# Kernel tuning notes

Hardware: AMD Instinct MI355X
Metric: run time of the kernel (lower is better)

The kernel has to match this reference:

```python
import jax, jax.numpy as jnp
import numpy as np

N_NODES = 50000
N_EDGES = 800000
IN_CH = 128
HID = 256
HEADS = 4
NEG_SLOPE = 0.2


def setup_inputs() -> dict:
    key = jax.random.key(0)
    ks = jax.random.split(key, 12)
    C1 = HID // HEADS  # 64 per head, layer 1
    inp = {
        "x": jax.random.normal(ks[0], (N_NODES, IN_CH), dtype=jnp.float32),
        "edge_index": jax.random.randint(ks[1], (2, N_EDGES), 0, N_NODES, dtype=jnp.int32),
        # layer 1: GATConv(128 -> 64, heads=4, concat=True)
        "W1": jax.random.normal(ks[2], (IN_CH, HEADS * C1), dtype=jnp.float32) * (1.0 / np.sqrt(IN_CH)),
        "a_src1": jax.random.normal(ks[3], (HEADS, C1), dtype=jnp.float32) * 0.1,
        "a_dst1": jax.random.normal(ks[4], (HEADS, C1), dtype=jnp.float32) * 0.1,
        "b1": jnp.zeros((HEADS * C1,), dtype=jnp.float32),
        # layer 2: GATConv(256 -> 256, heads=1, concat=False)
        "W2": jax.random.normal(ks[5], (HID, HID), dtype=jnp.float32) * (1.0 / np.sqrt(HID)),
        "a_src2": jax.random.normal(ks[6], (1, HID), dtype=jnp.float32) * 0.1,
        "a_dst2": jax.random.normal(ks[7], (1, HID), dtype=jnp.float32) * 0.1,
        "b2": jnp.zeros((HID,), dtype=jnp.float32),
    }
    return inp


def _gat_conv(x, src, dst, W, a_src, a_dst, H, C, n_nodes):
    """One PyG-style GATConv (eval mode, self-loops already appended)."""
    h = (x @ W).reshape(n_nodes, H, C)                      # [N,H,C]
    alpha_src = jnp.sum(h * a_src[None], axis=-1)           # [N,H]
    alpha_dst = jnp.sum(h * a_dst[None], axis=-1)           # [N,H]
    e = jax.nn.leaky_relu(alpha_src[src] + alpha_dst[dst], NEG_SLOPE)  # [E,H]
    # segment softmax over incoming edges of each dst node
    m = jax.ops.segment_max(e, dst, num_segments=n_nodes)  # [N,H]
    e = jnp.exp(e - m[dst])
    denom = jax.ops.segment_sum(e, dst, num_segments=n_nodes)
    alpha = e / (denom[dst] + 1e-16)                        # [E,H]
    msg = h[src] * alpha[:, :, None]                        # [E,H,C]
    return jax.ops.segment_sum(msg, dst, num_segments=n_nodes)  # [N,H,C]


def reference(x, edge_index, W1, a_src1, a_dst1, b1, W2, a_src2, a_dst2, b2):
    n = x.shape[0]
    loops = jnp.arange(n, dtype=edge_index.dtype)
    src = jnp.concatenate([edge_index[0], loops])
    dst = jnp.concatenate([edge_index[1], loops])
    C1 = HID // HEADS
    # layer 1: heads=4, concat -> [N, HID], then ELU (dropout inactive at eval)
    h1 = _gat_conv(x, src, dst, W1, a_src1, a_dst1, HEADS, C1, n)
    h1 = jax.nn.elu(h1.reshape(n, HEADS * C1) + b1)
    # layer 2: heads=1, concat=False -> mean over heads (trivial for H=1)
    h2 = _gat_conv(h1, src, dst, W2, a_src2, a_dst2, 1, HID, n)
    return h2.reshape(n, HID) + b2
```

## Files before the change

### kernel.cpp

```cpp
#include <hip/hip_runtime.h>
#include <hip/hip_fp16.h>

#define NNODES 50000
#define NEDGES 800000
#define HIDDIM 256
#define EN (NEDGES + NNODES)
#define NTILES ((NNODES + 63)/64)
#define NT64 (NTILES*64)
#define NPART 8

constexpr float NEG = 0.2f;

typedef __attribute__((ext_vector_type(8))) short short8_t;
typedef __attribute__((ext_vector_type(4))) float floatx4;

__device__ __forceinline__ float lrelu(float v){ return v >= 0.f ? v : NEG*v; }

__device__ __forceinline__ unsigned short bf16_rn(float x){
  unsigned u = __float_as_uint(x);
  return (unsigned short)((u + 0x7FFFu + ((u >> 16) & 1u)) >> 16);
}

__device__ __forceinline__ float4 ldh4(const __half* p){
  union { float2 f; __half2 h[2]; } u;
  u.f = *reinterpret_cast<const float2*>(p);
  const float2 lo = __half22float2(u.h[0]);
  const float2 hi = __half22float2(u.h[1]);
  return make_float4(lo.x, lo.y, hi.x, hi.y);
}

__global__ void k_count(const int* __restrict__ ei, int* counts, int E){
  int e = blockIdx.x*blockDim.x + threadIdx.x;
  if (e < E) atomicAdd(&counts[ei[E + e]], 1);
}

#define SCAN_CHUNK 2048
__global__ __launch_bounds__(256) void k_scan_a(const int* __restrict__ counts,
                                                int* __restrict__ bsum, int n){
  __shared__ int ws[4];
  const int t = threadIdx.x;
  const int idx0 = blockIdx.x*SCAN_CHUNK + t*8;
  int s = 0;
  #pragma unroll
  for (int i = 0; i < 8; ++i) if (idx0 + i < n) s += counts[idx0 + i] + 1;
  for (int off = 32; off; off >>= 1) s += __shfl_xor(s, off);
  if ((t & 63) == 0) ws[t >> 6] = s;
  __syncthreads();
  if (t == 0) bsum[blockIdx.x] = ws[0] + ws[1] + ws[2] + ws[3];
}
__global__ void k_scan_b(const int* __restrict__ bsum, int* __restrict__ boff,
                         int* __restrict__ offs, int nb, int n){
  if (threadIdx.x == 0){
    int run = 0;
    for (int i = 0; i < nb; ++i){ boff[i] = run; run += bsum[i]; }
    offs[n] = run;
  }
}
__global__ __launch_bounds__(256) void k_scan_c(const int* __restrict__ counts,
                                                const int* __restrict__ boff,
                                                int* __restrict__ offs,
                                                int* __restrict__ cursor, int n){
  __shared__ int sc[256];
  const int t = threadIdx.x;
  const int idx0 = blockIdx.x*SCAN_CHUNK + t*8;
  int v[8], pre[8], s = 0;
  #pragma unroll
  for (int i = 0; i < 8; ++i){
    v[i] = (idx0 + i < n) ? counts[idx0 + i] + 1 : 0;
    pre[i] = s; s += v[i];
  }
  sc[t] = s;
  __syncthreads();
  int run = s;
  for (int off = 1; off < 256; off <<= 1){
    int add = (t >= off) ? sc[t - off] : 0;
    __syncthreads();
    sc[t] += add;
    __syncthreads();
  }
  const int excl = sc[t] - run;
  const int toff = boff[blockIdx.x] + excl;
  #pragma unroll
  for (int i = 0; i < 8; ++i){
    if (idx0 + i < n){
      const int o = toff + pre[i];
      offs[idx0 + i] = o;
      cursor[idx0 + i] = o;
    }
  }
}

__global__ __launch_bounds__(256) void k_scatter(const int* __restrict__ ei, int* cursor,
                          int* __restrict__ esrc, int E, int n){
  const int part = blockIdx.x & (NPART-1);
  const int nchunk = gridDim.x >> 3;
  const int chunk = blockIdx.x >> 3;
  const int per = n / NPART;
  const int dlo = part*per, dhi = dlo + per;
  const int total = E + n;
  for (int e = chunk*256 + threadIdx.x; e < total; e += nchunk*256){
    const int d = (e < E) ? ei[E + e] : (e - E);
    if (d >= dlo && d < dhi){
      const int s = (e < E) ? ei[e] : d;
      esrc[atomicAdd(&cursor[d], 1)] = s;
    }
  }
}

__global__ __launch_bounds__(256) void k_wprep(
    const float* __restrict__ W1, const float* __restrict__ aS1, const float* __restrict__ aD1,
    const float* __restrict__ W2, const float* __restrict__ aS2, const float* __restrict__ aD2,
    unsigned short* __restrict__ W1hi, unsigned short* __restrict__ W1lo,
    unsigned short* __restrict__ W2hi, unsigned short* __restrict__ W2lo,
    float* __restrict__ va1, float* __restrict__ va2)
{
  const int b = blockIdx.x, t = threadIdx.x;
  if (b < 384){
    const float* W = (b < 128) ? W1 : W2;
    unsigned short* hi = (b < 128) ? W1hi : W2hi;
    unsigned short* lo = (b < 128) ? W1lo : W2lo;
    const int idx = ((b < 128) ? b : (b - 128))*256 + t;
    const int k = idx / HIDDIM, n = idx % HIDDIM;
    const float w = W[idx];
    const unsigned short h = bf16_rn(w);
    const unsigned short l = bf16_rn(w - __uint_as_float((unsigned)h << 16));
    const int p = ((k >> 3)*HIDDIM + n)*8 + (k & 7);
    hi[p] = h; lo[p] = l;
  } else {
    if (t < 128){
      #pragma unroll
      for (int h = 0; h < 4; ++h){
        float s = 0.f, d = 0.f;
        for (int k = 0; k < 64; ++k){
          const float w = W1[t*HIDDIM + h*64 + k];
          s = fmaf(w, aS1[h*64 + k], s);
          d = fmaf(w, aD1[h*64 + k], d);
        }
        va1[t*8 + h] = s;
        va1[t*8 + 4 + h] = d;
      }
    } else {
      for (int c = t - 128; c < 256; c += 128){
        float s = 0.f, d = 0.f;
        for (int j = 0; j < 256; ++j){
          const float w = W2[c*HIDDIM + j];
          s = fmaf(w, aS2[j], s);
          d = fmaf(w, aD2[j], d);
        }
        va2[c*2] = s; va2[c*2+1] = d;
      }
    }
  }
}

__global__ __launch_bounds__(256) void k_xh_logits(
    const float* __restrict__ X, const float* __restrict__ va1,
    __half* __restrict__ xh, float* __restrict__ as1, float* __restrict__ ad1, int n)
{
  const int lane = threadIdx.x & 63;
  const int node = blockIdx.x*4 + (threadIdx.x >> 6);
  if (node >= n) return;
  const float2 xv = *reinterpret_cast<const float2*>(X + (size_t)node*128 + 2*lane);
  *reinterpret_cast<__half2*>(xh + (size_t)node*128 + 2*lane) = __float22half2_rn(xv);

  const float4 vs0 = *reinterpret_cast<const float4*>(va1 + (2*lane)*8);
  const float4 vd0 = *reinterpret_cast<const float4*>(va1 + (2*lane)*8 + 4);
  const float4 vs1 = *reinterpret_cast<const float4*>(va1 + (2*lane+1)*8);
  const float4 vd1 = *reinterpret_cast<const float4*>(va1 + (2*lane+1)*8 + 4);
  float ps[4], pd[4];
  ps[0] = xv.x*vs0.x + xv.y*vs1.x;  pd[0] = xv.x*vd0.x + xv.y*vd1.x;
  ps[1] = xv.x*vs0.y + xv.y*vs1.y;  pd[1] = xv.x*vd0.y + xv.y*vd1.y;
  ps[2] = xv.x*vs0.z + xv.y*vs1.z;  pd[2] = xv.x*vd0.z + xv.y*vd1.z;
  ps[3] = xv.x*vs0.w + xv.y*vs1.w;  pd[3] = xv.x*vd0.w + xv.y*vd1.w;
  #pragma unroll
  for (int h = 0; h < 4; ++h)
    for (int off = 32; off; off >>= 1){
      ps[h] += __shfl_xor(ps[h], off);
      pd[h] += __shfl_xor(pd[h], off);
    }
  if (lane == 0){
    *reinterpret_cast<float4*>(as1 + (size_t)node*4) = make_float4(ps[0],ps[1],ps[2],ps[3]);
    *reinterpret_cast<float4*>(ad1 + (size_t)node*4) = make_float4(pd[0],pd[1],pd[2],pd[3]);
  }
}

template<int NH>
__global__ __launch_bounds__(256) void k_prep(
    const float* __restrict__ as_, const float* __restrict__ ad_,
    const int* __restrict__ offs, const int* __restrict__ esrc,
    __half* __restrict__ p16, float* __restrict__ rdinv, int n)
{
  constexpr float SHIFT = (NH == 4) ? 2.0f : 4.0f;
  const int lane = threadIdx.x & 63;
  const int node = blockIdx.x*4 + (threadIdx.x >> 6);
  if (node >= n) return;
  const int start = offs[node], end = offs[node+1];

  float adv[NH], dsum[NH];
  #pragma unroll
  for (int h = 0; h < NH; ++h){ adv[h] = ad_[node*NH + h] - SHIFT; dsum[h] = 0.f; }

  for (int e = start + lane; e < end; e += 64){
    const int s = esrc[e];
    if (NH == 4){
      const float4 av = *reinterpret_cast<const float4*>(as_ + (size_t)s*4);
      const float a[4] = {av.x, av.y, av.z, av.w};
      union { float2 f; __half2 h2[2]; } o;
      float wq[4];
      #pragma unroll
      for (int h = 0; h < 4; ++h){
        const __half w16 = __float2half(__expf(lrelu(a[h] + adv[h] + SHIFT) - SHIFT));
        wq[h] = __half2float(w16);
        dsum[h] += wq[h];
      }
      o.h2[0] = __half2{__float2half(wq[0]), __float2half(wq[1])};
      o.h2[1] = __half2{__float2half(wq[2]), __float2half(wq[3])};
      *reinterpret_cast<float2*>(&p16[(size_t)4*e]) = o.f;
    } else {
      const __half w16 = __float2half(__expf(lrelu(as_[s] + adv[0] + SHIFT) - SHIFT));
      p16[e] = w16;
      dsum[0] += __half2float(w16);
    }
  }
  #pragma unroll
  for (int h = 0; h < NH; ++h)
    for (int off = 32; off; off >>= 1) dsum[h] += __shfl_xor(dsum[h], off);

  if (lane == 0){
    if (NH == 4){
      *reinterpret_cast<float4*>(rdinv + (size_t)node*4) =
        make_float4(1.f/(dsum[0]+1e-16f), 1.f/(dsum[1]+1e-16f),
                    1.f/(dsum[2]+1e-16f), 1.f/(dsum[3]+1e-16f));
    } else {
      rdinv[node] = 1.f/(dsum[0]+1e-16f);
    }
  }
}

__global__ __launch_bounds__(256) void k_agg1(
    const __half* __restrict__ xh, const __half* __restrict__ p16,
    const int* __restrict__ offs, const int* __restrict__ esrc,
    const float* __restrict__ rdinv, unsigned short* __restrict__ xagg, int n)
{
  const int l2 = threadIdx.x & 31;
  const int node = blockIdx.x*8 + (threadIdx.x >> 5);
  if (node >= n) return;
  const int start = offs[node], end = offs[node+1];
  const __half* hp = xh + 4*l2;

  float acc[4][4] = {};
  int e = start;
  for (; e + 8 <= end; e += 8){
    int s[8]; float2 pv[8]; float2 xv[8];
    #pragma unroll
    for (int i = 0; i < 8; ++i) s[i] = esrc[e+i];
    #pragma unroll
    for (int i = 0; i < 8; ++i) pv[i] = *reinterpret_cast<const float2*>(p16 + (size_t)4*(e+i));
    #pragma unroll
    for (int i = 0; i < 8; ++i) xv[i] = *reinterpret_cast<const float2*>(hp + (size_t)s[i]*128);
    #pragma unroll
    for (int i = 0; i < 8; ++i){
      union { float2 f; __half2 h2[2]; } ux; ux.f = xv[i];
      const float2 x01 = __half22float2(ux.h2[0]);
      const float2 x23 = __half22float2(ux.h2[1]);
      union { float2 f; __half2 h2[2]; } up; up.f = pv[i];
      const float2 p01 = __half22float2(up.h2[0]);
      const float2 p23 = __half22float2(up.h2[1]);
      const float ph[4] = {p01.x, p01.y, p23.x, p23.y};
      const float xc[4] = {x01.x, x01.y, x23.x, x23.y};
      #pragma unroll
      for (int h = 0; h < 4; ++h)
        #pragma unroll
        for (int c = 0; c < 4; ++c)
          acc[h][c] = fmaf(ph[h], xc[c], acc[h][c]);
    }
  }
  for (; e < end; ++e){
    const int s = esrc[e];
    union { float2 f; __half2 h2[2]; } ux;
    ux.f = *reinterpret_cast<const float2*>(hp + (size_t)s*128);
    const float2 x01 = __half22float2(ux.h2[0]);
    const float2 x23 = __half22float2(ux.h2[1]);
    union { float2 f; __half2 h2[2]; } up;
    up.f = *reinterpret_cast<const float2*>(p16 + (size_t)4*e);
    const float2 p01 = __half22float2(up.h2[0]);
    const float2 p23 = __half22float2(up.h2[1]);
    const float ph[4] = {p01.x, p01.y, p23.x, p23.y};
    const float xc[4] = {x01.x, x01.y, x23.x, x23.y};
    #pragma unroll
    for (int h = 0; h < 4; ++h)
      #pragma unroll
      for (int c = 0; c < 4; ++c)
        acc[h][c] = fmaf(ph[h], xc[c], acc[h][c]);
  }
  const float4 rv = *reinterpret_cast<const float4*>(rdinv + (size_t)node*4);
  const float rd[4] = {rv.x, rv.y, rv.z, rv.w};
  #pragma unroll
  for (int h = 0; h < 4; ++h){
    uint2 pk;
    pk.x = (unsigned)bf16_rn(acc[h][0]*rd[h]) | ((unsigned)bf16_rn(acc[h][1]*rd[h]) << 16);
    pk.y = (unsigned)bf16_rn(acc[h][2]*rd[h]) | ((unsigned)bf16_rn(acc[h][3]*rd[h]) << 16);
    *reinterpret_cast<uint2*>(xagg + (size_t)node*512 + h*128 + 4*l2) = pk;
  }
}

__global__ __launch_bounds__(256) void k_gemm1(
    const unsigned short* __restrict__ Xagg,
    const unsigned short* __restrict__ Bhi, const unsigned short* __restrict__ Blo,
    const float* __restrict__ b1, const float* __restrict__ va2,
    __half* __restrict__ h1e, float* __restrict__ as2, float* __restrict__ ad2, int M)
{
  __shared__ float lred_s[64][4], lred_d[64][4];
  const int tid = threadIdx.x;
  const int w = tid >> 6, l = tid & 63;
  const int lr = l & 15, lg = l >> 4;
  const int row0 = blockIdx.x*64;
  const int n0 = w*64;
  floatx4 acc[4][4] = {};

  for (int ks = 0; ks < 4; ++ks){
    short8_t a_[4], bh[4], bl[4];
    #pragma unroll
    for (int m = 0; m < 4; ++m){
      const size_t ao = (size_t)(row0 + 16*m + lr)*512 + w*128 + ks*32 + lg*8;
      a_[m] = *reinterpret_cast<const short8_t*>(&Xagg[ao]);
    }
    #pragma unroll
    for (int n = 0; n < 4; ++n){
      const int boff = (((ks*4 + lg)*HIDDIM) + n0 + 16*n + lr)*8;
      bh[n] = *reinterpret_cast<const short8_t*>(&Bhi[boff]);
      bl[n] = *reinterpret_cast<const short8_t*>(&Blo[boff]);
    }
    #pragma unroll
    for (int m = 0; m < 4; ++m)
      #pragma unroll
      for (int n = 0; n < 4; ++n){
        acc[m][n] = __builtin_amdgcn_mfma_f32_16x16x32_bf16(a_[m], bh[n], acc[m][n], 0,0,0);
        acc[m][n] = __builtin_amdgcn_mfma_f32_16x16x32_bf16(a_[m], bl[n], acc[m][n], 0,0,0);
      }
  }

  float bcol[4], v2s[4], v2d[4];
  #pragma unroll
  for (int n = 0; n < 4; ++n){
    const int col = n0 + 16*n + lr;
    bcol[n] = b1[col];
    v2s[n] = va2[col*2];
    v2d[n] = va2[col*2+1];
  }
  #pragma unroll
  for (int m = 0; m < 4; ++m){
    #pragma unroll
    for (int r = 0; r < 4; ++r){
      const int row = row0 + 16*m + lg*4 + r;
      float ps = 0.f, pd = 0.f;
      #pragma unroll
      for (int n = 0; n < 4; ++n){
        float v = acc[m][n][r] + bcol[n];
        v = v > 0.f ? v : __expf(v) - 1.f;
        if (row < M) h1e[(size_t)row*HIDDIM + n0 + 16*n + lr] = __float2half(v);
        ps = fmaf(v, v2s[n], ps);
        pd = fmaf(v, v2d[n], pd);
      }
      #pragma unroll
      for (int off = 1; off <= 8; off <<= 1){
        ps += __shfl_xor(ps, off);
        pd += __shfl_xor(pd, off);
      }
      const int rloc = 16*m + lg*4 + r;
      if (lr == 0){ lred_s[rloc][w] = ps; lred_d[rloc][w] = pd; }
    }
  }
  __syncthreads();
  if (tid < 64 && row0 + tid < M){
    as2[row0+tid] = lred_s[tid][0]+lred_s[tid][1]+lred_s[tid][2]+lred_s[tid][3];
    ad2[row0+tid] = lred_d[tid][0]+lred_d[tid][1]+lred_d[tid][2]+lred_d[tid][3];
  }
}

__global__ __launch_bounds__(256) void k_agg2(
    const __half* __restrict__ Hs, const __half* __restrict__ p16,
    const int* __restrict__ offs, const int* __restrict__ esrc,
    const float* __restrict__ rdinv, unsigned short* __restrict__ xagg2, int n)
{
  const int lane = threadIdx.x & 63;
  const int node = blockIdx.x*4 + (threadIdx.x >> 6);
  if (node >= n) return;
  const int start = offs[node], end = offs[node+1];
  const __half* hp = Hs + 4*lane;

  float4 a0 = {0,0,0,0}, a1 = {0,0,0,0}, a2 = {0,0,0,0}, a3 = {0,0,0,0};
  int e = start;
  for (; e + 8 <= end; e += 8){
    int s[8]; float pw[8]; float4 hv[8];
    #pragma unroll
    for (int i = 0; i < 8; ++i) s[i] = esrc[e+i];
    #pragma unroll
    for (int i = 0; i < 8; ++i) pw[i] = __half2float(p16[e+i]);
    #pragma unroll
    for (int i = 0; i < 8; ++i) hv[i] = ldh4(hp + (size_t)s[i]*HIDDIM);
    #pragma unroll
    for (int i = 0; i < 8; i += 4){
      a0.x = fmaf(pw[i+0], hv[i+0].x, a0.x); a0.y = fmaf(pw[i+0], hv[i+0].y, a0.y);
      a0.z = fmaf(pw[i+0], hv[i+0].z, a0.z); a0.w = fmaf(pw[i+0], hv[i+0].w, a0.w);
      a1.x = fmaf(pw[i+1], hv[i+1].x, a1.x); a1.y = fmaf(pw[i+1], hv[i+1].y, a1.y);
      a1.z = fmaf(pw[i+1], hv[i+1].z, a1.z); a1.w = fmaf(pw[i+1], hv[i+1].w, a1.w);
      a2.x = fmaf(pw[i+2], hv[i+2].x, a2.x); a2.y = fmaf(pw[i+2], hv[i+2].y, a2.y);
      a2.z = fmaf(pw[i+2], hv[i+2].z, a2.z); a2.w = fmaf(pw[i+2], hv[i+2].w, a2.w);
      a3.x = fmaf(pw[i+3], hv[i+3].x, a3.x); a3.y = fmaf(pw[i+3], hv[i+3].y, a3.y);
      a3.z = fmaf(pw[i+3], hv[i+3].z, a3.z); a3.w = fmaf(pw[i+3], hv[i+3].w, a3.w);
    }
  }
  for (; e < end; ++e){
    const int s = esrc[e];
    const float p = __half2float(p16[e]);
    const float4 hv = ldh4(hp + (size_t)s*HIDDIM);
    a0.x = fmaf(p, hv.x, a0.x); a0.y = fmaf(p, hv.y, a0.y);
    a0.z = fmaf(p, hv.z, a0.z); a0.w = fmaf(p, hv.w, a0.w);
  }
  const float rd = rdinv[node];
  float4 acc;
  acc.x = ((a0.x + a1.x) + (a2.x + a3.x)) * rd;
  acc.y = ((a0.y + a1.y) + (a2.y + a3.y)) * rd;
  acc.z = ((a0.z + a1.z) + (a2.z + a3.z)) * rd;
  acc.w = ((a0.w + a1.w) + (a2.w + a3.w)) * rd;

  uint2 pk;
  pk.x = (unsigned)bf16_rn(acc.x) | ((unsigned)bf16_rn(acc.y) << 16);
  pk.y = (unsigned)bf16_rn(acc.z) | ((unsigned)bf16_rn(acc.w) << 16);
  *reinterpret_cast<uint2*>(xagg2 + (size_t)node*HIDDIM + 4*lane) = pk;
}

__global__ __launch_bounds__(256) void k_gemm2(
    const unsigned short* __restrict__ Xagg2,
    const unsigned short* __restrict__ Bhi, const unsigned short* __restrict__ Blo,
    const float* __restrict__ b2, float* __restrict__ Out, int M)
{
  const int tid = threadIdx.x;
  const int w = tid >> 6, l = tid & 63;
  const int lr = l & 15, lg = l >> 4;
  const int row0 = blockIdx.x*64;
  const int n0 = w*64;
  floatx4 acc[4][4] = {};

  for (int ks = 0; ks < 8; ++ks){
    short8_t a_[4], bh[4], bl[4];
    #pragma unroll
    for (int m = 0; m < 4; ++m){
      const size_t ao = (size_t)(row0 + 16*m + lr)*HIDDIM + ks*32 + lg*8;
      a_[m] = *reinterpret_cast<const short8_t*>(&Xagg2[ao]);
    }
    #pragma unroll
    for (int n = 0; n < 4; ++n){
      const int boff = (((ks*4 + lg)*HIDDIM) + n0 + 16*n + lr)*8;
      bh[n] = *reinterpret_cast<const short8_t*>(&Bhi[boff]);
      bl[n] = *reinterpret_cast<const short8_t*>(&Blo[boff]);
    }
    #pragma unroll
    for (int m = 0; m < 4; ++m)
      #pragma unroll
      for (int n = 0; n < 4; ++n){
        acc[m][n] = __builtin_amdgcn_mfma_f32_16x16x32_bf16(a_[m], bh[n], acc[m][n], 0,0,0);
        acc[m][n] = __builtin_amdgcn_mfma_f32_16x16x32_bf16(a_[m], bl[n], acc[m][n], 0,0,0);
      }
  }

  float bcol[4];
  #pragma unroll
  for (int n = 0; n < 4; ++n) bcol[n] = b2[n0 + 16*n + lr];
  #pragma unroll
  for (int m = 0; m < 4; ++m){
    #pragma unroll
    for (int r = 0; r < 4; ++r){
      const int row = row0 + 16*m + lg*4 + r;
      if (row < M){
        #pragma unroll
        for (int n = 0; n < 4; ++n)
          Out[(size_t)row*HIDDIM + n0 + 16*n + lr] = acc[m][n][r] + bcol[n];
      }
    }
  }
}

extern "C" void kernel_launch(void* const* d_in, const int* in_sizes, int n_in,
                              void* d_out, int out_size, void* d_ws, size_t ws_size,
                              hipStream_t stream)
{
  const float* x    = (const float*)d_in[0];
  const int*   ei   = (const int*)  d_in[1];
  const float* W1   = (const float*)d_in[2];
  const float* aS1  = (const float*)d_in[3];
  const float* aD1  = (const float*)d_in[4];
  const float* b1   = (const float*)d_in[5];
  const float* W2   = (const float*)d_in[6];
  const float* aS2  = (const float*)d_in[7];
  const float* aD2  = (const float*)d_in[8];
  const float* b2   = (const float*)d_in[9];
  float* out = (float*)d_out;

  char* ws = (char*)d_ws;
  size_t off = 0;
  auto alloc = [&](size_t bytes){ void* p = ws + off; off += (bytes + 255) & ~255ull; return p; };

  unsigned short* xagg  = (unsigned short*)alloc((size_t)NT64*512*sizeof(short));
  __half*         h1e   = (__half*)alloc((size_t)NT64*HIDDIM*sizeof(__half));
  unsigned short* xagg2 = (unsigned short*)alloc((size_t)NT64*HIDDIM*sizeof(short));
  __half*         xh    = (__half*)xagg2;
  __half* p16   = (__half*)alloc((size_t)4*EN*sizeof(__half));
  float* as1    = (float*)alloc((size_t)NNODES*4*sizeof(float));
  float* ad1    = (float*)alloc((size_t)NNODES*4*sizeof(float));
  float* rdinv1 = (float*)alloc((size_t)NNODES*4*sizeof(float));
  float* as2    = (float*)alloc((size_t)NNODES*sizeof(float));
  float* ad2    = (float*)alloc((size_t)NNODES*sizeof(float));
  float* rdinv2 = (float*)alloc((size_t)NNODES*sizeof(float));
  float* va1    = (float*)alloc(128*8*sizeof(float));
  float* va2    = (float*)alloc(256*2*sizeof(float));
  unsigned short* W1hi = (unsigned short*)alloc((size_t)128*HIDDIM*sizeof(short));
  unsigned short* W1lo = (unsigned short*)alloc((size_t)128*HIDDIM*sizeof(short));
  unsigned short* W2hi = (unsigned short*)alloc((size_t)256*HIDDIM*sizeof(short));
  unsigned short* W2lo = (unsigned short*)alloc((size_t)256*HIDDIM*sizeof(short));
  int*   counts = (int*)alloc((size_t)NNODES*sizeof(int));
  int*   offs   = (int*)alloc((size_t)(NNODES+1)*sizeof(int));
  int*   cursor = (int*)alloc((size_t)NNODES*sizeof(int));
  int*   bsum   = (int*)alloc(64*sizeof(int));
  int*   boff   = (int*)alloc(64*sizeof(int));
  int*   esrc   = (int*)alloc((size_t)EN*sizeof(int));

  const int nscan = (NNODES + SCAN_CHUNK - 1)/SCAN_CHUNK;
  const int node_grid = (NNODES + 3)/4;

  hipMemsetAsync(counts, 0, (size_t)NNODES*sizeof(int), stream);
  k_count     <<<(NEDGES+255)/256, 256, 0, stream>>>(ei, counts, NEDGES);
  k_scan_a    <<<nscan, 256, 0, stream>>>(counts, bsum, NNODES);
  k_scan_b    <<<1, 64, 0, stream>>>(bsum, boff, offs, nscan, NNODES);
  k_scan_c    <<<nscan, 256, 0, stream>>>(counts, boff, offs, cursor, NNODES);
  k_scatter   <<<NPART*120, 256, 0, stream>>>(ei, cursor, esrc, NEDGES, NNODES);

  k_wprep<<<385, 256, 0, stream>>>(W1, aS1, aD1, W2, aS2, aD2,
                                   W1hi, W1lo, W2hi, W2lo, va1, va2);
  k_xh_logits<<<node_grid, 256, 0, stream>>>(x, va1, xh, as1, ad1, NNODES);

  k_prep<4><<<node_grid, 256, 0, stream>>>(as1, ad1, offs, esrc, p16, rdinv1, NNODES);
  k_agg1<<<(NNODES+7)/8, 256, 0, stream>>>(xh, p16, offs, esrc, rdinv1, xagg, NNODES);
  k_gemm1<<<NTILES, 256, 0, stream>>>(xagg, W1hi, W1lo, b1, va2, h1e, as2, ad2, NNODES);

  k_prep<1><<<node_grid, 256, 0, stream>>>(as2, ad2, offs, esrc, p16, rdinv2, NNODES);
  k_agg2<<<node_grid, 256, 0, stream>>>(h1e, p16, offs, esrc, rdinv2, xagg2, NNODES);
  k_gemm2<<<NTILES, 256, 0, stream>>>(xagg2, W2hi, W2lo, b2, out, NNODES);
}
```

Measured before the change: 344.8 us.

## Split layer-2 aggregation into feature slabs with 16 lanes per node

Layer-2 aggregation is reorganized so that each block handles one 32-column feature slab (of 8) for 16 nodes, with 16 lanes per node each loading a half2, instead of one wavefront per node loading 4 halves per lane. Consecutive blocks share a node group across slabs, so each slab's gathered rows form a smaller working set. The goal is better cache locality for the random gathers. The cost is that edge indices and weights are re-read 8 times and each load is narrower (4 bytes instead of 8), which adds memory instructions.

```diff
diff --git a/kernel.cpp b/kernel.cpp
--- a/kernel.cpp
+++ b/kernel.cpp
@@ -19,14 +19,6 @@
 __device__ __forceinline__ unsigned short bf16_rn(float x){
   unsigned u = __float_as_uint(x);
   return (unsigned short)((u + 0x7FFFu + ((u >> 16) & 1u)) >> 16);
-}
-
-__device__ __forceinline__ float4 ldh4(const __half* p){
-  union { float2 f; __half2 h[2]; } u;
-  u.f = *reinterpret_cast<const float2*>(p);
-  const float2 lo = __half22float2(u.h[0]);
-  const float2 hi = __half22float2(u.h[1]);
-  return make_float4(lo.x, lo.y, hi.x, hi.y);
 }
 
 __global__ void k_count(const int* __restrict__ ei, int* counts, int E){
@@ -383,52 +375,46 @@
     const int* __restrict__ offs, const int* __restrict__ esrc,
     const float* __restrict__ rdinv, unsigned short* __restrict__ xagg2, int n)
 {
-  const int lane = threadIdx.x & 63;
-  const int node = blockIdx.x*4 + (threadIdx.x >> 6);
+  const int slab = blockIdx.x & 7;
+  const int l4 = threadIdx.x & 15;
+  const int node = (blockIdx.x >> 3)*16 + (threadIdx.x >> 4);
   if (node >= n) return;
   const int start = offs[node], end = offs[node+1];
-  const __half* hp = Hs + 4*lane;
-
-  float4 a0 = {0,0,0,0}, a1 = {0,0,0,0}, a2 = {0,0,0,0}, a3 = {0,0,0,0};
+  const __half* hp = Hs + slab*32 + 2*l4;
+
+  float a0x=0.f,a0y=0.f,a1x=0.f,a1y=0.f,a2x=0.f,a2y=0.f,a3x=0.f,a3y=0.f;
   int e = start;
   for (; e + 8 <= end; e += 8){
-    int s[8]; float pw[8]; float4 hv[8];
+    int s[8]; float pw[8]; __half2 hv[8];
     #pragma unroll
     for (int i = 0; i < 8; ++i) s[i] = esrc[e+i];
     #pragma unroll
     for (int i = 0; i < 8; ++i) pw[i] = __half2float(p16[e+i]);
     #pragma unroll
-    for (int i = 0; i < 8; ++i) hv[i] = ldh4(hp + (size_t)s[i]*HIDDIM);
+    for (int i = 0; i < 8; ++i) hv[i] = *reinterpret_cast<const __half2*>(hp + (size_t)s[i]*HIDDIM);
     #pragma unroll
     for (int i = 0; i < 8; i += 4){
-      a0.x = fmaf(pw[i+0], hv[i+0].x, a0.x); a0.y = fmaf(pw[i+0], hv[i+0].y, a0.y);
-      a0.z = fmaf(pw[i+0], hv[i+0].z, a0.z); a0.w = fmaf(pw[i+0], hv[i+0].w, a0.w);
-      a1.x = fmaf(pw[i+1], hv[i+1].x, a1.x); a1.y = fmaf(pw[i+1], hv[i+1].y, a1.y);
-      a1.z = fmaf(pw[i+1], hv[i+1].z, a1.z); a1.w = fmaf(pw[i+1], hv[i+1].w, a1.w);
-      a2.x = fmaf(pw[i+2], hv[i+2].x, a2.x); a2.y = fmaf(pw[i+2], hv[i+2].y, a2.y);
-      a2.z = fmaf(pw[i+2], hv[i+2].z, a2.z); a2.w = fmaf(pw[i+2], hv[i+2].w, a2.w);
-      a3.x = fmaf(pw[i+3], hv[i+3].x, a3.x); a3.y = fmaf(pw[i+3], hv[i+3].y, a3.y);
-      a3.z = fmaf(pw[i+3], hv[i+3].z, a3.z); a3.w = fmaf(pw[i+3], hv[i+3].w, a3.w);
+      const float2 f0 = __half22float2(hv[i+0]);
+      const float2 f1 = __half22float2(hv[i+1]);
+      const float2 f2 = __half22float2(hv[i+2]);
+      const float2 f3 = __half22float2(hv[i+3]);
+      a0x = fmaf(pw[i+0], f0.x, a0x); a0y = fmaf(pw[i+0], f0.y, a0y);
+      a1x = fmaf(pw[i+1], f1.x, a1x); a1y = fmaf(pw[i+1], f1.y, a1y);
+      a2x = fmaf(pw[i+2], f2.x, a2x); a2y = fmaf(pw[i+2], f2.y, a2y);
+      a3x = fmaf(pw[i+3], f3.x, a3x); a3y = fmaf(pw[i+3], f3.y, a3y);
     }
   }
   for (; e < end; ++e){
     const int s = esrc[e];
     const float p = __half2float(p16[e]);
-    const float4 hv = ldh4(hp + (size_t)s*HIDDIM);
-    a0.x = fmaf(p, hv.x, a0.x); a0.y = fmaf(p, hv.y, a0.y);
-    a0.z = fmaf(p, hv.z, a0.z); a0.w = fmaf(p, hv.w, a0.w);
+    const float2 f = __half22float2(*reinterpret_cast<const __half2*>(hp + (size_t)s*HIDDIM));
+    a0x = fmaf(p, f.x, a0x); a0y = fmaf(p, f.y, a0y);
   }
   const float rd = rdinv[node];
-  float4 acc;
-  acc.x = ((a0.x + a1.x) + (a2.x + a3.x)) * rd;
-  acc.y = ((a0.y + a1.y) + (a2.y + a3.y)) * rd;
-  acc.z = ((a0.z + a1.z) + (a2.z + a3.z)) * rd;
-  acc.w = ((a0.w + a1.w) + (a2.w + a3.w)) * rd;
-
-  uint2 pk;
-  pk.x = (unsigned)bf16_rn(acc.x) | ((unsigned)bf16_rn(acc.y) << 16);
-  pk.y = (unsigned)bf16_rn(acc.z) | ((unsigned)bf16_rn(acc.w) << 16);
-  *reinterpret_cast<uint2*>(xagg2 + (size_t)node*HIDDIM + 4*lane) = pk;
+  const float rx = ((a0x + a1x) + (a2x + a3x)) * rd;
+  const float ry = ((a0y + a1y) + (a2y + a3y)) * rd;
+  const unsigned pk = (unsigned)bf16_rn(rx) | ((unsigned)bf16_rn(ry) << 16);
+  *reinterpret_cast<unsigned*>(xagg2 + (size_t)node*HIDDIM + slab*32 + 2*l4) = pk;
 }
 
 __global__ __launch_bounds__(256) void k_gemm2(
@@ -545,6 +531,6 @@
   k_gemm1<<<NTILES, 256, 0, stream>>>(xagg, W1hi, W1lo, b1, va2, h1e, as2, ad2, NNODES);
 
   k_prep<1><<<node_grid, 256, 0, stream>>>(as2, ad2, offs, esrc, p16, rdinv2, NNODES);
-  k_agg2<<<node_grid, 256, 0, stream>>>(h1e, p16, offs, esrc, rdinv2, xagg2, NNODES);
+  k_agg2<<<8*((NNODES+15)/16), 256, 0, stream>>>(h1e, p16, offs, esrc, rdinv2, xagg2, NNODES);
   k_gemm2<<<NTILES, 256, 0, stream>>>(xagg2, W2hi, W2lo, b2, out, NNODES);
 }
```

After: 384.6 us. 1.12x slower.

## Fuse layer-2 softmax weights into aggregation, narrow prep groups, partition count atomics

Applied to the files above, without the earlier changes.

Layer-2 edge weights and their normaliser are now computed inside k_agg2, so the separate k_prep<1> pass and its p16/rdinv2 round trip are gone. The weight exp is recomputed redundantly across the 64 lanes of each wave, and the gather unroll drops from 8 to 4. Layer-1 prep now uses 16 lanes per node instead of 64 to suit the average degree of about 17. k_count partitions destination ranges across blocks to localise atomics, at the cost of each block rereading the edge list.

```diff
diff --git a/kernel.cpp b/kernel.cpp
--- a/kernel.cpp
+++ b/kernel.cpp
@@ -29,9 +29,17 @@
   return make_float4(lo.x, lo.y, hi.x, hi.y);
 }
 
-__global__ void k_count(const int* __restrict__ ei, int* counts, int E){
-  int e = blockIdx.x*blockDim.x + threadIdx.x;
-  if (e < E) atomicAdd(&counts[ei[E + e]], 1);
+__global__ __launch_bounds__(256) void k_count(const int* __restrict__ ei,
+                                               int* counts, int E, int n){
+  const int part = blockIdx.x & (NPART-1);
+  const int nchunk = gridDim.x >> 3;
+  const int chunk = blockIdx.x >> 3;
+  const int per = n / NPART;
+  const int dlo = part*per, dhi = dlo + per;
+  for (int e = chunk*256 + threadIdx.x; e < E; e += nchunk*256){
+    const int d = ei[E + e];
+    if (d >= dlo && d < dhi) atomicAdd(&counts[d], 1);
+  }
 }
 
 #define SCAN_CHUNK 2048
@@ -184,56 +192,45 @@
   }
 }
 
-template<int NH>
-__global__ __launch_bounds__(256) void k_prep(
+__global__ __launch_bounds__(256) void k_prep4(
     const float* __restrict__ as_, const float* __restrict__ ad_,
     const int* __restrict__ offs, const int* __restrict__ esrc,
     __half* __restrict__ p16, float* __restrict__ rdinv, int n)
 {
-  constexpr float SHIFT = (NH == 4) ? 2.0f : 4.0f;
-  const int lane = threadIdx.x & 63;
-  const int node = blockIdx.x*4 + (threadIdx.x >> 6);
+  constexpr float SHIFT = 2.0f;
+  const int l4 = threadIdx.x & 15;
+  const int node = blockIdx.x*16 + (threadIdx.x >> 4);
   if (node >= n) return;
   const int start = offs[node], end = offs[node+1];
 
-  float adv[NH], dsum[NH];
-  #pragma unroll
-  for (int h = 0; h < NH; ++h){ adv[h] = ad_[node*NH + h] - SHIFT; dsum[h] = 0.f; }
-
-  for (int e = start + lane; e < end; e += 64){
+  const float4 adv4 = *reinterpret_cast<const float4*>(ad_ + (size_t)node*4);
+  const float adv[4] = {adv4.x, adv4.y, adv4.z, adv4.w};
+  float dsum[4] = {0.f, 0.f, 0.f, 0.f};
+
+  for (int e = start + l4; e < end; e += 16){
     const int s = esrc[e];
-    if (NH == 4){
-      const float4 av = *reinterpret_cast<const float4*>(as_ + (size_t)s*4);
-      const float a[4] = {av.x, av.y, av.z, av.w};
-      union { float2 f; __half2 h2[2]; } o;
-      float wq[4];
-      #pragma unroll
-      for (int h = 0; h < 4; ++h){
-        const __half w16 = __float2half(__expf(lrelu(a[h] + adv[h] + SHIFT) - SHIFT));
-        wq[h] = __half2float(w16);
-        dsum[h] += wq[h];
-      }
-      o.h2[0] = __half2{__float2half(wq[0]), __float2half(wq[1])};
-      o.h2[1] = __half2{__float2half(wq[2]), __float2half(wq[3])};
-      *reinterpret_cast<float2*>(&p16[(size_t)4*e]) = o.f;
-    } else {
-      const __half w16 = __float2half(__expf(lrelu(as_[s] + adv[0] + SHIFT) - SHIFT));
-      p16[e] = w16;
-      dsum[0] += __half2float(w16);
-    }
-  }
-  #pragma unroll
-  for (int h = 0; h < NH; ++h)
-    for (int off = 32; off; off >>= 1) dsum[h] += __shfl_xor(dsum[h], off);
-
-  if (lane == 0){
-    if (NH == 4){
-      *reinterpret_cast<float4*>(rdinv + (size_t)node*4) =
-        make_float4(1.f/(dsum[0]+1e-16f), 1.f/(dsum[1]+1e-16f),
-                    1.f/(dsum[2]+1e-16f), 1.f/(dsum[3]+1e-16f));
-    } else {
-      rdinv[node] = 1.f/(dsum[0]+1e-16f);
-    }
+    const float4 av = *reinterpret_cast<const float4*>(as_ + (size_t)s*4);
+    const float a[4] = {av.x, av.y, av.z, av.w};
+    union { float2 f; __half2 h2[2]; } o;
+    float wq[4];
+    #pragma unroll
+    for (int h = 0; h < 4; ++h){
+      const __half w16 = __float2half(__expf(lrelu(a[h] + adv[h]) - SHIFT));
+      wq[h] = __half2float(w16);
+      dsum[h] += wq[h];
+    }
+    o.h2[0] = __half2{__float2half(wq[0]), __float2half(wq[1])};
+    o.h2[1] = __half2{__float2half(wq[2]), __float2half(wq[3])};
+    *reinterpret_cast<float2*>(&p16[(size_t)4*e]) = o.f;
+  }
+  #pragma unroll
+  for (int h = 0; h < 4; ++h)
+    for (int off = 8; off; off >>= 1) dsum[h] += __shfl_xor(dsum[h], off);
+
+  if (l4 == 0){
+    *reinterpret_cast<float4*>(rdinv + (size_t)node*4) =
+      make_float4(1.f/(dsum[0]+1e-16f), 1.f/(dsum[1]+1e-16f),
+                  1.f/(dsum[2]+1e-16f), 1.f/(dsum[3]+1e-16f));
   }
 }
 
@@ -379,46 +376,51 @@
 }
 
 __global__ __launch_bounds__(256) void k_agg2(
-    const __half* __restrict__ Hs, const __half* __restrict__ p16,
+    const __half* __restrict__ Hs,
+    const float* __restrict__ as2, const float* __restrict__ ad2,
     const int* __restrict__ offs, const int* __restrict__ esrc,
-    const float* __restrict__ rdinv, unsigned short* __restrict__ xagg2, int n)
-{
+    unsigned short* __restrict__ xagg2, int n)
+{
+  constexpr float SHIFT = 4.0f;
   const int lane = threadIdx.x & 63;
   const int node = blockIdx.x*4 + (threadIdx.x >> 6);
   if (node >= n) return;
   const int start = offs[node], end = offs[node+1];
+  const float adn = ad2[node];
   const __half* hp = Hs + 4*lane;
 
   float4 a0 = {0,0,0,0}, a1 = {0,0,0,0}, a2 = {0,0,0,0}, a3 = {0,0,0,0};
+  float dsum = 0.f;
   int e = start;
-  for (; e + 8 <= end; e += 8){
-    int s[8]; float pw[8]; float4 hv[8];
-    #pragma unroll
-    for (int i = 0; i < 8; ++i) s[i] = esrc[e+i];
-    #pragma unroll
-    for (int i = 0; i < 8; ++i) pw[i] = __half2float(p16[e+i]);
-    #pragma unroll
-    for (int i = 0; i < 8; ++i) hv[i] = ldh4(hp + (size_t)s[i]*HIDDIM);
-    #pragma unroll
-    for (int i = 0; i < 8; i += 4){
-      a0.x = fmaf(pw[i+0], hv[i+0].x, a0.x); a0.y = fmaf(pw[i+0], hv[i+0].y, a0.y);
-      a0.z = fmaf(pw[i+0], hv[i+0].z, a0.z); a0.w = fmaf(pw[i+0], hv[i+0].w, a0.w);
-      a1.x = fmaf(pw[i+1], hv[i+1].x, a1.x); a1.y = fmaf(pw[i+1], hv[i+1].y, a1.y);
-      a1.z = fmaf(pw[i+1], hv[i+1].z, a1.z); a1.w = fmaf(pw[i+1], hv[i+1].w, a1.w);
-      a2.x = fmaf(pw[i+2], hv[i+2].x, a2.x); a2.y = fmaf(pw[i+2], hv[i+2].y, a2.y);
-      a2.z = fmaf(pw[i+2], hv[i+2].z, a2.z); a2.w = fmaf(pw[i+2], hv[i+2].w, a2.w);
-      a3.x = fmaf(pw[i+3], hv[i+3].x, a3.x); a3.y = fmaf(pw[i+3], hv[i+3].y, a3.y);
-      a3.z = fmaf(pw[i+3], hv[i+3].z, a3.z); a3.w = fmaf(pw[i+3], hv[i+3].w, a3.w);
-    }
+  for (; e + 4 <= end; e += 4){
+    const int s0 = esrc[e+0], s1 = esrc[e+1], s2 = esrc[e+2], s3 = esrc[e+3];
+    const float w0 = __expf(lrelu(as2[s0] + adn) - SHIFT);
+    const float w1 = __expf(lrelu(as2[s1] + adn) - SHIFT);
+    const float w2 = __expf(lrelu(as2[s2] + adn) - SHIFT);
+    const float w3 = __expf(lrelu(as2[s3] + adn) - SHIFT);
+    dsum += (w0 + w1) + (w2 + w3);
+    const float4 h0 = ldh4(hp + (size_t)s0*HIDDIM);
+    const float4 h1 = ldh4(hp + (size_t)s1*HIDDIM);
+    const float4 h2 = ldh4(hp + (size_t)s2*HIDDIM);
+    const float4 h3 = ldh4(hp + (size_t)s3*HIDDIM);
+    a0.x = fmaf(w0, h0.x, a0.x); a0.y = fmaf(w0, h0.y, a0.y);
+    a0.z = fmaf(w0, h0.z, a0.z); a0.w = fmaf(w0, h0.w, a0.w);
+    a1.x = fmaf(w1, h1.x, a1.x); a1.y = fmaf(w1, h1.y, a1.y);
+    a1.z = fmaf(w1, h1.z, a1.z); a1.w = fmaf(w1, h1.w, a1.w);
+    a2.x = fmaf(w2, h2.x, a2.x); a2.y = fmaf(w2, h2.y, a2.y);
+    a2.z = fmaf(w2, h2.z, a2.z); a2.w = fmaf(w2, h2.w, a2.w);
+    a3.x = fmaf(w3, h3.x, a3.x); a3.y = fmaf(w3, h3.y, a3.y);
+    a3.z = fmaf(w3, h3.z, a3.z); a3.w = fmaf(w3, h3.w, a3.w);
   }
   for (; e < end; ++e){
     const int s = esrc[e];
-    const float p = __half2float(p16[e]);
+    const float w = __expf(lrelu(as2[s] + adn) - SHIFT);
+    dsum += w;
     const float4 hv = ldh4(hp + (size_t)s*HIDDIM);
-    a0.x = fmaf(p, hv.x, a0.x); a0.y = fmaf(p, hv.y, a0.y);
-    a0.z = fmaf(p, hv.z, a0.z); a0.w = fmaf(p, hv.w, a0.w);
-  }
-  const float rd = rdinv[node];
+    a0.x = fmaf(w, hv.x, a0.x); a0.y = fmaf(w, hv.y, a0.y);
+    a0.z = fmaf(w, hv.z, a0.z); a0.w = fmaf(w, hv.w, a0.w);
+  }
+  const float rd = 1.f/(dsum + 1e-16f);
   float4 acc;
   acc.x = ((a0.x + a1.x) + (a2.x + a3.x)) * rd;
   acc.y = ((a0.y + a1.y) + (a2.y + a3.y)) * rd;
@@ -512,7 +514,6 @@
   float* rdinv1 = (float*)alloc((size_t)NNODES*4*sizeof(float));
   float* as2    = (float*)alloc((size_t)NNODES*sizeof(float));
   float* ad2    = (float*)alloc((size_t)NNODES*sizeof(float));
-  float* rdinv2 = (float*)alloc((size_t)NNODES*sizeof(float));
   float* va1    = (float*)alloc(128*8*sizeof(float));
   float* va2    = (float*)alloc(256*2*sizeof(float));
   unsigned short* W1hi = (unsigned short*)alloc((size_t)128*HIDDIM*sizeof(short));
@@ -530,7 +531,7 @@
   const int node_grid = (NNODES + 3)/4;
 
   hipMemsetAsync(counts, 0, (size_t)NNODES*sizeof(int), stream);
-  k_count     <<<(NEDGES+255)/256, 256, 0, stream>>>(ei, counts, NEDGES);
+  k_count     <<<NPART*120, 256, 0, stream>>>(ei, counts, NEDGES, NNODES);
   k_scan_a    <<<nscan, 256, 0, stream>>>(counts, bsum, NNODES);
   k_scan_b    <<<1, 64, 0, stream>>>(bsum, boff, offs, nscan, NNODES);
   k_scan_c    <<<nscan, 256, 0, stream>>>(counts, boff, offs, cursor, NNODES);
@@ -540,11 +541,10 @@
                                    W1hi, W1lo, W2hi, W2lo, va1, va2);
   k_xh_logits<<<node_grid, 256, 0, stream>>>(x, va1, xh, as1, ad1, NNODES);
 
-  k_prep<4><<<node_grid, 256, 0, stream>>>(as1, ad1, offs, esrc, p16, rdinv1, NNODES);
+  k_prep4<<<(NNODES+15)/16, 256, 0, stream>>>(as1, ad1, offs, esrc, p16, rdinv1, NNODES);
   k_agg1<<<(NNODES+7)/8, 256, 0, stream>>>(xh, p16, offs, esrc, rdinv1, xagg, NNODES);
   k_gemm1<<<NTILES, 256, 0, stream>>>(xagg, W1hi, W1lo, b1, va2, h1e, as2, ad2, NNODES);
 
-  k_prep<1><<<node_grid, 256, 0, stream>>>(as2, ad2, offs, esrc, p16, rdinv2, NNODES);
-  k_agg2<<<node_grid, 256, 0, stream>>>(h1e, p16, offs, esrc, rdinv2, xagg2, NNODES);
+  k_agg2<<<node_grid, 256, 0, stream>>>(h1e, as2, ad2, offs, esrc, xagg2, NNODES);
   k_gemm2<<<NTILES, 256, 0, stream>>>(xagg2, W2hi, W2lo, b2, out, NNODES);
 }
```

New measurement: 322.2 us (median of 2 runs). 6.6% less time.
